# Kernel tuning notes

Hardware: AMD Instinct MI355X
Metric: run time of the kernel (lower is better)

## Reference

```python
import jax, jax.numpy as jnp
import numpy as np

B, T, C, H = 4096, 64, 128, 64  # batch, seq (== blok_olcusu), embed (yerlesdirme_olcusu), head size


def setup_inputs() -> dict:
    key = jax.random.key(0)
    kx, kq, kk, kv = jax.random.split(key, 4)
    x = jax.random.normal(kx, (B, T, C), dtype=jnp.float32)
    # Linear(C, H, bias=False); stored as [in, out] so projection is x @ W
    Wq = jax.random.normal(kq, (C, H), dtype=jnp.float32) * (C ** -0.5)
    Wk = jax.random.normal(kk, (C, H), dtype=jnp.float32) * (C ** -0.5)
    Wv = jax.random.normal(kv, (C, H), dtype=jnp.float32) * (C ** -0.5)
    return {"x": x, "Wq": Wq, "Wk": Wk, "Wv": Wv}


def reference(x, Wq, Wk, Wv):
    _, t, c = x.shape
    q = jnp.einsum("btc,ch->bth", x, Wq)
    k = jnp.einsum("btc,ch->bth", x, Wk)
    v = jnp.einsum("btc,ch->bth", x, Wv)
    # NOTE: source scales by C**-0.5 where C is the EMBEDDING dim, not head size
    scores = jnp.einsum("bth,bsh->bts", q, k) * (c ** -0.5)  # [B, T, T]
    causal = jnp.tril(jnp.ones((t, t), dtype=bool))
    scores = jnp.where(causal, scores, -jnp.inf)
    attn = jax.nn.softmax(scores, axis=-1)
    # dropout is identity in eval mode
    out = jnp.einsum("bts,bsh->bth", attn, v)  # [B, T, H]
    return out
```

## Files before the change

### kernel.cpp

```cpp
#include <hip/hip_runtime.h>
#include <stdint.h>

#define NB 4096
#define TT 64
#define CC 128
#define HH 64

#define WSTR 136
#define QSTR 72

typedef __bf16 bf16x8 __attribute__((ext_vector_type(8)));
typedef float f32x4 __attribute__((ext_vector_type(4)));

__device__ __forceinline__ unsigned short f2bf(float f) {
  union { float f; uint32_t u; } a; a.f = f;
  uint32_t u = a.u;
  u += 0x7fffu + ((u >> 16) & 1u);
  return (unsigned short)(u >> 16);
}

__global__ void transpose_w_kernel(const float* __restrict__ Wq,
                                   const float* __restrict__ Wk,
                                   const float* __restrict__ Wv,
                                   unsigned short* __restrict__ wT) {
  int i = blockIdx.x * 256 + threadIdx.x;
  if (i >= 3 * CC * HH) return;
  int mat = i / (CC * HH);
  int r   = i % (CC * HH);
  int c   = r / HH;
  int h   = r % HH;
  const float* W = (mat == 0) ? Wq : (mat == 1) ? Wk : Wv;
  wT[mat * (CC * HH) + h * CC + c] = f2bf(W[c * HH + h]);
}

__global__ __launch_bounds__(256, 2)
void attn_kernel(const float* __restrict__ x,
                 const unsigned short* __restrict__ wT,
                 float* __restrict__ out) {
  __shared__ unsigned short wbuf[64 * WSTR];
  __shared__ unsigned short qs[64 * QSTR];
  __shared__ unsigned short ks[64 * QSTR];
  __shared__ unsigned short vts[64 * QSTR];

  const int b    = blockIdx.x;
  const int tid  = threadIdx.x;
  const int wave = tid >> 6;
  const int lane = tid & 63;
  const int quad = lane >> 4;
  const int l15  = lane & 15;
  const int mbase = wave * 16;

  bf16x8 xfrag[4];
  {
    const float* xr = x + ((size_t)b * TT + mbase + l15) * CC + quad * 8;
    #pragma unroll
    for (int ks_ = 0; ks_ < 4; ++ks_) {
      f32x4 lo = *(const f32x4*)(xr + ks_ * 32);
      f32x4 hi = *(const f32x4*)(xr + ks_ * 32 + 4);
      bf16x8 f;
      #pragma unroll
      for (int j = 0; j < 4; ++j) {
        union { unsigned short u; __bf16 b; } cv;
        cv.u = f2bf(lo[j]); f[j] = cv.b;
        cv.u = f2bf(hi[j]); f[j + 4] = cv.b;
      }
      xfrag[ks_] = f;
    }
  }

  #pragma unroll
  for (int mat = 0; mat < 3; ++mat) {
    const unsigned short* wsrc = wT + mat * (CC * HH);
    #pragma unroll
    for (int r = 0; r < 4; ++r) {
      int flat = (r * 256 + tid) * 8;
      int row  = flat >> 7;
      int col  = flat & 127;
      *(uint4*)(&wbuf[row * WSTR + col]) = *(const uint4*)(wsrc + flat);
    }
    __syncthreads();

    #pragma unroll
    for (int nt = 0; nt < 4; ++nt) {
      f32x4 acc = {0.f, 0.f, 0.f, 0.f};
      #pragma unroll
      for (int ks_ = 0; ks_ < 4; ++ks_) {
        bf16x8 bfrag = *(const bf16x8*)(&wbuf[(nt * 16 + l15) * WSTR + ks_ * 32 + quad * 8]);
        acc = __builtin_amdgcn_mfma_f32_16x16x32_bf16(xfrag[ks_], bfrag, acc, 0, 0, 0);
      }
      #pragma unroll
      for (int r = 0; r < 4; ++r) {
        int row = mbase + quad * 4 + r;
        int col = nt * 16 + l15;
        unsigned short v = f2bf(acc[r]);
        if (mat == 0)      qs[row * QSTR + col] = v;
        else if (mat == 1) ks[row * QSTR + col] = v;
        else               vts[col * QSTR + row] = v;
      }
    }
    __syncthreads();
  }

  f32x4 sc[4];
  {
    bf16x8 aq[2];
    #pragma unroll
    for (int k2 = 0; k2 < 2; ++k2)
      aq[k2] = *(const bf16x8*)(&qs[(mbase + l15) * QSTR + k2 * 32 + quad * 8]);
    #pragma unroll
    for (int nt = 0; nt < 4; ++nt) {
      f32x4 acc = {0.f, 0.f, 0.f, 0.f};
      #pragma unroll
      for (int k2 = 0; k2 < 2; ++k2) {
        bf16x8 bk = *(const bf16x8*)(&ks[(nt * 16 + l15) * QSTR + k2 * 32 + quad * 8]);
        acc = __builtin_amdgcn_mfma_f32_16x16x32_bf16(aq[k2], bk, acc, 0, 0, 0);
      }
      sc[nt] = acc;
    }
  }
  const float scale = 0.08838834764831845f;
  #pragma unroll
  for (int r = 0; r < 4; ++r) {
    int row = mbase + quad * 4 + r;
    float vals[4];
    #pragma unroll
    for (int nt = 0; nt < 4; ++nt) {
      int col = nt * 16 + l15;
      float v = sc[nt][r] * scale;
      vals[nt] = (col <= row) ? v : -__builtin_inff();
    }
    float m = fmaxf(fmaxf(vals[0], vals[1]), fmaxf(vals[2], vals[3]));
    #pragma unroll
    for (int d = 1; d < 16; d <<= 1) m = fmaxf(m, __shfl_xor(m, d, 64));
    float s = 0.f;
    #pragma unroll
    for (int nt = 0; nt < 4; ++nt) { vals[nt] = __expf(vals[nt] - m); s += vals[nt]; }
    #pragma unroll
    for (int d = 1; d < 16; d <<= 1) s += __shfl_xor(s, d, 64);
    float inv = 1.f / s;
    #pragma unroll
    for (int nt = 0; nt < 4; ++nt)
      wbuf[row * WSTR + nt * 16 + l15] = f2bf(vals[nt] * inv);
  }
  __syncthreads();

  bf16x8 ap[2];
  #pragma unroll
  for (int k2 = 0; k2 < 2; ++k2)
    ap[k2] = *(const bf16x8*)(&wbuf[(mbase + l15) * WSTR + k2 * 32 + quad * 8]);
  float* ob = out + ((size_t)b * TT) * HH;
  #pragma unroll
  for (int nt = 0; nt < 4; ++nt) {
    f32x4 acc = {0.f, 0.f, 0.f, 0.f};
    #pragma unroll
    for (int k2 = 0; k2 < 2; ++k2) {
      bf16x8 bv = *(const bf16x8*)(&vts[(nt * 16 + l15) * QSTR + k2 * 32 + quad * 8]);
      acc = __builtin_amdgcn_mfma_f32_16x16x32_bf16(ap[k2], bv, acc, 0, 0, 0);
    }
    #pragma unroll
    for (int r = 0; r < 4; ++r) {
      int row = mbase + quad * 4 + r;
      ob[row * HH + nt * 16 + l15] = acc[r];
    }
  }
}

extern "C" void kernel_launch(void* const* d_in, const int* in_sizes, int n_in,
                              void* d_out, int out_size, void* d_ws, size_t ws_size,
                              hipStream_t stream) {
  const float* x  = (const float*)d_in[0];
  const float* Wq = (const float*)d_in[1];
  const float* Wk = (const float*)d_in[2];
  const float* Wv = (const float*)d_in[3];
  unsigned short* wT = (unsigned short*)d_ws;
  float* outp = (float*)d_out;

  transpose_w_kernel<<<(3 * CC * HH + 255) / 256, 256, 0, stream>>>(Wq, Wk, Wv, wT);
  attn_kernel<<<NB, 256, 0, stream>>>(x, wT, outp);
}
```

Measured before the change: 228.1 us.

## Pre-swizzle weights into MFMA fragment order and process four batches per block

Weights are pre-arranged into per-lane MFMA fragment order, so each wave loads B fragments straight from global/L2 and the shared-memory weight staging and its barriers go away. Each block now loops over four batch elements, and the softmax probabilities reuse the Q buffer instead of a separate one. Launch bounds rise to four blocks per CU since LDS use drops. The trade-off is that weights are re-read from cache per batch and there are fewer blocks (1024) to fill the GPU.

```diff
diff --git a/kernel.cpp b/kernel.cpp
--- a/kernel.cpp
+++ b/kernel.cpp
@@ -5,8 +5,7 @@
 #define TT 64
 #define CC 128
 #define HH 64
-
-#define WSTR 136
+#define BPB 4
 #define QSTR 72
 
 typedef __bf16 bf16x8 __attribute__((ext_vector_type(8)));
@@ -19,148 +18,150 @@
   return (unsigned short)(u >> 16);
 }
 
-__global__ void transpose_w_kernel(const float* __restrict__ Wq,
-                                   const float* __restrict__ Wk,
-                                   const float* __restrict__ Wv,
-                                   unsigned short* __restrict__ wT) {
+__global__ void swizzle_w_kernel(const float* __restrict__ Wq,
+                                 const float* __restrict__ Wk,
+                                 const float* __restrict__ Wv,
+                                 unsigned short* __restrict__ wz) {
   int i = blockIdx.x * 256 + threadIdx.x;
-  if (i >= 3 * CC * HH) return;
-  int mat = i / (CC * HH);
-  int r   = i % (CC * HH);
-  int c   = r / HH;
-  int h   = r % HH;
+  if (i >= 3 * 16 * 64) return;
+  int mat  = i >> 10;
+  int rem  = i & 1023;
+  int frag = rem >> 6;
+  int lane = rem & 63;
+  int nt = frag >> 2, ks = frag & 3;
+  int quad = lane >> 4, l15 = lane & 15;
+  int h  = nt * 16 + l15;
+  int c0 = ks * 32 + quad * 8;
   const float* W = (mat == 0) ? Wq : (mat == 1) ? Wk : Wv;
-  wT[mat * (CC * HH) + h * CC + c] = f2bf(W[c * HH + h]);
+  unsigned short* o = wz + (size_t)i * 8;
+  #pragma unroll
+  for (int j = 0; j < 8; ++j) o[j] = f2bf(W[(c0 + j) * HH + h]);
 }
 
-__global__ __launch_bounds__(256, 2)
+__global__ __launch_bounds__(256, 4)
 void attn_kernel(const float* __restrict__ x,
-                 const unsigned short* __restrict__ wT,
+                 const unsigned short* __restrict__ wz,
                  float* __restrict__ out) {
-  __shared__ unsigned short wbuf[64 * WSTR];
   __shared__ unsigned short qs[64 * QSTR];
-  __shared__ unsigned short ks[64 * QSTR];
+  __shared__ unsigned short ks_[64 * QSTR];
   __shared__ unsigned short vts[64 * QSTR];
 
-  const int b    = blockIdx.x;
   const int tid  = threadIdx.x;
   const int wave = tid >> 6;
   const int lane = tid & 63;
   const int quad = lane >> 4;
   const int l15  = lane & 15;
   const int mbase = wave * 16;
+  const float scale = 0.08838834764831845f;
 
-  bf16x8 xfrag[4];
-  {
-    const float* xr = x + ((size_t)b * TT + mbase + l15) * CC + quad * 8;
+  const int b0 = blockIdx.x * BPB;
+
+  for (int bi = 0; bi < BPB; ++bi) {
+    const int b = b0 + bi;
+
+    bf16x8 xfrag[4];
+    {
+      const float* xr = x + ((size_t)b * TT + mbase + l15) * CC + quad * 8;
+      #pragma unroll
+      for (int ksi = 0; ksi < 4; ++ksi) {
+        f32x4 lo = *(const f32x4*)(xr + ksi * 32);
+        f32x4 hi = *(const f32x4*)(xr + ksi * 32 + 4);
+        bf16x8 f;
+        #pragma unroll
+        for (int j = 0; j < 4; ++j) {
+          union { unsigned short u; __bf16 b; } cv;
+          cv.u = f2bf(lo[j]); f[j] = cv.b;
+          cv.u = f2bf(hi[j]); f[j + 4] = cv.b;
+        }
+        xfrag[ksi] = f;
+      }
+    }
+
+    if (bi > 0) __syncthreads();
+
     #pragma unroll
-    for (int ks_ = 0; ks_ < 4; ++ks_) {
-      f32x4 lo = *(const f32x4*)(xr + ks_ * 32);
-      f32x4 hi = *(const f32x4*)(xr + ks_ * 32 + 4);
-      bf16x8 f;
+    for (int mat = 0; mat < 3; ++mat) {
+      const unsigned short* wm = wz + mat * (16 * 64 * 8);
       #pragma unroll
-      for (int j = 0; j < 4; ++j) {
-        union { unsigned short u; __bf16 b; } cv;
-        cv.u = f2bf(lo[j]); f[j] = cv.b;
-        cv.u = f2bf(hi[j]); f[j + 4] = cv.b;
+      for (int nt = 0; nt < 4; ++nt) {
+        f32x4 acc = {0.f, 0.f, 0.f, 0.f};
+        #pragma unroll
+        for (int ksi = 0; ksi < 4; ++ksi) {
+          bf16x8 bfrag = *(const bf16x8*)(wm + (((nt * 4 + ksi) * 64) + lane) * 8);
+          acc = __builtin_amdgcn_mfma_f32_16x16x32_bf16(xfrag[ksi], bfrag, acc, 0, 0, 0);
+        }
+        #pragma unroll
+        for (int r = 0; r < 4; ++r) {
+          int row = mbase + quad * 4 + r;
+          int col = nt * 16 + l15;
+          unsigned short v = f2bf(acc[r]);
+          if (mat == 0)      qs[row * QSTR + col] = v;
+          else if (mat == 1) ks_[row * QSTR + col] = v;
+          else               vts[col * QSTR + row] = v;
+        }
       }
-      xfrag[ks_] = f;
-    }
-  }
-
-  #pragma unroll
-  for (int mat = 0; mat < 3; ++mat) {
-    const unsigned short* wsrc = wT + mat * (CC * HH);
-    #pragma unroll
-    for (int r = 0; r < 4; ++r) {
-      int flat = (r * 256 + tid) * 8;
-      int row  = flat >> 7;
-      int col  = flat & 127;
-      *(uint4*)(&wbuf[row * WSTR + col]) = *(const uint4*)(wsrc + flat);
     }
     __syncthreads();
 
-    #pragma unroll
-    for (int nt = 0; nt < 4; ++nt) {
-      f32x4 acc = {0.f, 0.f, 0.f, 0.f};
+    f32x4 sc[4];
+    {
+      bf16x8 aq[2];
       #pragma unroll
-      for (int ks_ = 0; ks_ < 4; ++ks_) {
-        bf16x8 bfrag = *(const bf16x8*)(&wbuf[(nt * 16 + l15) * WSTR + ks_ * 32 + quad * 8]);
-        acc = __builtin_amdgcn_mfma_f32_16x16x32_bf16(xfrag[ks_], bfrag, acc, 0, 0, 0);
-      }
+      for (int k2 = 0; k2 < 2; ++k2)
+        aq[k2] = *(const bf16x8*)(&qs[(mbase + l15) * QSTR + k2 * 32 + quad * 8]);
       #pragma unroll
-      for (int r = 0; r < 4; ++r) {
-        int row = mbase + quad * 4 + r;
-        int col = nt * 16 + l15;
-        unsigned short v = f2bf(acc[r]);
-        if (mat == 0)      qs[row * QSTR + col] = v;
-        else if (mat == 1) ks[row * QSTR + col] = v;
-        else               vts[col * QSTR + row] = v;
+      for (int nt = 0; nt < 4; ++nt) {
+        f32x4 acc = {0.f, 0.f, 0.f, 0.f};
+        #pragma unroll
+        for (int k2 = 0; k2 < 2; ++k2) {
+          bf16x8 bk = *(const bf16x8*)(&ks_[(nt * 16 + l15) * QSTR + k2 * 32 + quad * 8]);
+          acc = __builtin_amdgcn_mfma_f32_16x16x32_bf16(aq[k2], bk, acc, 0, 0, 0);
+        }
+        sc[nt] = acc;
       }
     }
-    __syncthreads();
-  }
+    #pragma unroll
+    for (int r = 0; r < 4; ++r) {
+      int row = mbase + quad * 4 + r;
+      float vals[4];
+      #pragma unroll
+      for (int nt = 0; nt < 4; ++nt) {
+        int col = nt * 16 + l15;
+        float v = sc[nt][r] * scale;
+        vals[nt] = (col <= row) ? v : -__builtin_inff();
+      }
+      float m = fmaxf(fmaxf(vals[0], vals[1]), fmaxf(vals[2], vals[3]));
+      #pragma unroll
+      for (int d = 1; d < 16; d <<= 1) m = fmaxf(m, __shfl_xor(m, d, 64));
+      float s = 0.f;
+      #pragma unroll
+      for (int nt = 0; nt < 4; ++nt) { vals[nt] = __expf(vals[nt] - m); s += vals[nt]; }
+      #pragma unroll
+      for (int d = 1; d < 16; d <<= 1) s += __shfl_xor(s, d, 64);
+      float inv = 1.f / s;
+      #pragma unroll
+      for (int nt = 0; nt < 4; ++nt)
+        qs[row * QSTR + nt * 16 + l15] = f2bf(vals[nt] * inv);
+    }
 
-  f32x4 sc[4];
-  {
-    bf16x8 aq[2];
+    bf16x8 ap[2];
     #pragma unroll
     for (int k2 = 0; k2 < 2; ++k2)
-      aq[k2] = *(const bf16x8*)(&qs[(mbase + l15) * QSTR + k2 * 32 + quad * 8]);
+      ap[k2] = *(const bf16x8*)(&qs[(mbase + l15) * QSTR + k2 * 32 + quad * 8]);
+    float* ob = out + ((size_t)b * TT) * HH;
     #pragma unroll
     for (int nt = 0; nt < 4; ++nt) {
       f32x4 acc = {0.f, 0.f, 0.f, 0.f};
       #pragma unroll
       for (int k2 = 0; k2 < 2; ++k2) {
-        bf16x8 bk = *(const bf16x8*)(&ks[(nt * 16 + l15) * QSTR + k2 * 32 + quad * 8]);
-        acc = __builtin_amdgcn_mfma_f32_16x16x32_bf16(aq[k2], bk, acc, 0, 0, 0);
+        bf16x8 bv = *(const bf16x8*)(&vts[(nt * 16 + l15) * QSTR + k2 * 32 + quad * 8]);
+        acc = __builtin_amdgcn_mfma_f32_16x16x32_bf16(ap[k2], bv, acc, 0, 0, 0);
       }
-      sc[nt] = acc;
-    }
-  }
-  const float scale = 0.08838834764831845f;
-  #pragma unroll
-  for (int r = 0; r < 4; ++r) {
-    int row = mbase + quad * 4 + r;
-    float vals[4];
-    #pragma unroll
-    for (int nt = 0; nt < 4; ++nt) {
-      int col = nt * 16 + l15;
-      float v = sc[nt][r] * scale;
-      vals[nt] = (col <= row) ? v : -__builtin_inff();
-    }
-    float m = fmaxf(fmaxf(vals[0], vals[1]), fmaxf(vals[2], vals[3]));
-    #pragma unroll
-    for (int d = 1; d < 16; d <<= 1) m = fmaxf(m, __shfl_xor(m, d, 64));
-    float s = 0.f;
-    #pragma unroll
-    for (int nt = 0; nt < 4; ++nt) { vals[nt] = __expf(vals[nt] - m); s += vals[nt]; }
-    #pragma unroll
-    for (int d = 1; d < 16; d <<= 1) s += __shfl_xor(s, d, 64);
-    float inv = 1.f / s;
-    #pragma unroll
-    for (int nt = 0; nt < 4; ++nt)
-      wbuf[row * WSTR + nt * 16 + l15] = f2bf(vals[nt] * inv);
-  }
-  __syncthreads();
-
-  bf16x8 ap[2];
-  #pragma unroll
-  for (int k2 = 0; k2 < 2; ++k2)
-    ap[k2] = *(const bf16x8*)(&wbuf[(mbase + l15) * WSTR + k2 * 32 + quad * 8]);
-  float* ob = out + ((size_t)b * TT) * HH;
-  #pragma unroll
-  for (int nt = 0; nt < 4; ++nt) {
-    f32x4 acc = {0.f, 0.f, 0.f, 0.f};
-    #pragma unroll
-    for (int k2 = 0; k2 < 2; ++k2) {
-      bf16x8 bv = *(const bf16x8*)(&vts[(nt * 16 + l15) * QSTR + k2 * 32 + quad * 8]);
-      acc = __builtin_amdgcn_mfma_f32_16x16x32_bf16(ap[k2], bv, acc, 0, 0, 0);
-    }
-    #pragma unroll
-    for (int r = 0; r < 4; ++r) {
-      int row = mbase + quad * 4 + r;
-      ob[row * HH + nt * 16 + l15] = acc[r];
+      #pragma unroll
+      for (int r = 0; r < 4; ++r) {
+        int row = mbase + quad * 4 + r;
+        ob[row * HH + nt * 16 + l15] = acc[r];
+      }
     }
   }
 }
@@ -172,9 +173,9 @@
   const float* Wq = (const float*)d_in[1];
   const float* Wk = (const float*)d_in[2];
   const float* Wv = (const float*)d_in[3];
-  unsigned short* wT = (unsigned short*)d_ws;
+  unsigned short* wz = (unsigned short*)d_ws;
   float* outp = (float*)d_out;
 
-  transpose_w_kernel<<<(3 * CC * HH + 255) / 256, 256, 0, stream>>>(Wq, Wk, Wv, wT);
-  attn_kernel<<<NB, 256, 0, stream>>>(x, wT, outp);
+  swizzle_w_kernel<<<(3 * 16 * 64 + 255) / 256, 256, 0, stream>>>(Wq, Wk, Wv, wz);
+  attn_kernel<<<NB / BPB, 256, 0, stream>>>(x, wz, outp);
 }
```

New measurement: 315.7 us. +38.4%, slower.
